# Optimization experiments

Measured on AMD Instinct MI355X. Metric: run time of the kernel, lower is better.

Reference implementation:

```python
import jax, jax.numpy as jnp
import numpy as np

B, C, D, M = 256, 1024, 512, 4096
EPS = 1e-12  # F.normalize default eps


def setup_inputs() -> dict:
    key = jax.random.key(0)
    k1, k2 = jax.random.split(key)
    feature = jax.random.normal(k1, (B, C, D), dtype=jnp.float32)
    memory = jax.random.normal(k2, (M, C), dtype=jnp.float32)
    mask = jnp.ones((B,), dtype=bool)
    return {"feature": feature, "memory": memory, "mask": mask, "train": 1}


def reference(feature, memory, mask, train):
    # ---- Global_Pattern_Adjustment ----
    attn = jax.nn.softmax(feature.mean(axis=1), axis=-1)            # [B, D]
    feature_G = (feature * attn[:, None, :]).mean(axis=-1)          # [B, C]
    score = feature_G @ memory.T                                    # [B, M]
    score_memory = jax.nn.softmax(score, axis=0)                    # softmax over batch
    score_image = jax.nn.softmax(score, axis=1)                     # softmax over memory slots
    memory_response = jax.lax.stop_gradient(score_image) @ memory   # [B, C]
    memory_response = feature_G + memory_response
    global_compensation = feature + memory_response[:, :, None]     # [B, C, D]

    if not train:
        return global_compensation

    # ---- Memory_Evolution (mask-filtered rows emulated by zeroing their update) ----
    idx = jnp.argmax(score_image, axis=1)                           # topk(k=1) -> [B]
    weights = jnp.take_along_axis(score_memory, idx[:, None], axis=1)  # [B, 1]
    m = mask.astype(feature.dtype)[:, None]                         # [B, 1]
    update_vector = feature_G * weights * m                         # [B, C]
    increment = jnp.zeros_like(memory).at[idx].add(update_vector)   # scatter_add -> [M, C]
    upd = increment + memory
    norm = jnp.maximum(jnp.linalg.norm(upd, axis=1, keepdims=True), EPS)
    updated_memory = jax.lax.stop_gradient(upd / norm)              # [M, C]
    return (global_compensation, updated_memory)
```

## Files before the change

### kernel.cpp

```cpp
#include <hip/hip_runtime.h>
#include <math.h>

#define B 256
#define C 1024
#define D 512
#define M 4096
#define KS_SC 4
#define KS_MR 16
#define CHUNK 64
#define CPB 32
#define NCP (C / CPB)
static constexpr float EPS = 1e-12f;

typedef float fx4 __attribute__((ext_vector_type(4)));

__global__ __launch_bounds__(256) void k_colmean(const float* __restrict__ f,
                                                 float* __restrict__ colpart, int b0) {
    __shared__ fx4 buf[128];
    int bx = blockIdx.x, cc = blockIdx.y;
    int b = b0 + bx;
    int t = threadIdx.x;
    int r = t >> 7, lane = t & 127;
    const fx4* f4 = reinterpret_cast<const fx4*>(f)
                  + ((size_t)b * C + cc * CPB + r * 16) * (D / 4) + lane;
    fx4 acc = (fx4)(0.f);
#pragma unroll
    for (int k = 0; k < 16; ++k) acc += f4[(size_t)k * (D / 4)];
    if (r) buf[lane] = acc;
    __syncthreads();
    if (!r) {
        acc += buf[lane];
        reinterpret_cast<fx4*>(colpart)[((size_t)cc * CHUNK + bx) * (D / 4) + lane] = acc;
    }
}

__global__ __launch_bounds__(256) void k_attn(const float* __restrict__ colpart,
                                              float* __restrict__ attnD, int b0) {
    __shared__ float red[256];
    int bl = blockIdx.x;
    int b = b0 + bl;
    int t = threadIdx.x;
    float s0 = 0.f, s1 = 0.f;
#pragma unroll
    for (int p = 0; p < NCP; ++p) {
        s0 += colpart[((size_t)p * CHUNK + bl) * D + t];
        s1 += colpart[((size_t)p * CHUNK + bl) * D + t + 256];
    }
    float x0 = s0 * (1.0f / C), x1 = s1 * (1.0f / C);
    red[t] = fmaxf(x0, x1); __syncthreads();
    for (int s = 128; s > 0; s >>= 1) {
        if (t < s) red[t] = fmaxf(red[t], red[t + s]);
        __syncthreads();
    }
    float mx = red[0]; __syncthreads();
    float e0 = expf(x0 - mx), e1 = expf(x1 - mx);
    red[t] = e0 + e1; __syncthreads();
    for (int s = 128; s > 0; s >>= 1) {
        if (t < s) red[t] += red[t + s];
        __syncthreads();
    }
    float inv = 1.0f / (red[0] * (float)D);
    attnD[(size_t)b * D + t] = e0 * inv;
    attnD[(size_t)b * D + t + 256] = e1 * inv;
}

__global__ __launch_bounds__(256) void k_fg(const float* __restrict__ f,
                                            const float* __restrict__ attnD,
                                            float* __restrict__ fG, int b0) {
    int w = blockIdx.x * 4 + (threadIdx.x >> 6);
    int lane = threadIdx.x & 63;
    int b = b0 + (w >> 10);
    int c = w & 1023;
    const float4* f4 = reinterpret_cast<const float4*>(f) + ((size_t)b * C + c) * (D / 4);
    const float4* a4 = reinterpret_cast<const float4*>(attnD) + (size_t)b * (D / 4);
    float4 v0 = f4[lane], v1 = f4[lane + 64];
    float4 a0 = a4[lane], a1 = a4[lane + 64];
    float acc = v0.x * a0.x + v0.y * a0.y + v0.z * a0.z + v0.w * a0.w
              + v1.x * a1.x + v1.y * a1.y + v1.z * a1.z + v1.w * a1.w;
    for (int s = 32; s > 0; s >>= 1) acc += __shfl_xor(acc, s, 64);
    if (lane == 0) fG[(size_t)b * C + c] = acc;
}

__global__ __launch_bounds__(256) void k_score(const float* __restrict__ A,
                                               const float* __restrict__ Bm,
                                               float* __restrict__ score_p) {
    __shared__ float As[16][64];
    __shared__ float Bs[16][64];
    int t = threadIdx.x;
    int brow = blockIdx.y * 64;
    int mcol = blockIdx.x * 64;
    int kc0 = blockIdx.z * (C / KS_SC);
    int lr = t >> 2, lq = t & 3;
    int r0 = (t >> 4) << 2, c0 = (t & 15) << 2;
    float acc[4][4] = {};
    for (int kc = kc0; kc < kc0 + C / KS_SC; kc += 16) {
        float4 av = *reinterpret_cast<const float4*>(A + (size_t)(brow + lr) * C + kc + lq * 4);
        float4 bv = *reinterpret_cast<const float4*>(Bm + (size_t)(mcol + lr) * C + kc + lq * 4);
        __syncthreads();
        As[lq * 4 + 0][lr] = av.x; As[lq * 4 + 1][lr] = av.y;
        As[lq * 4 + 2][lr] = av.z; As[lq * 4 + 3][lr] = av.w;
        Bs[lq * 4 + 0][lr] = bv.x; Bs[lq * 4 + 1][lr] = bv.y;
        Bs[lq * 4 + 2][lr] = bv.z; Bs[lq * 4 + 3][lr] = bv.w;
        __syncthreads();
#pragma unroll
        for (int kk = 0; kk < 16; ++kk) {
            float a[4], bb[4];
#pragma unroll
            for (int i = 0; i < 4; ++i) a[i] = As[kk][r0 + i];
#pragma unroll
            for (int j = 0; j < 4; ++j) bb[j] = Bs[kk][c0 + j];
#pragma unroll
            for (int i = 0; i < 4; ++i)
#pragma unroll
                for (int j = 0; j < 4; ++j) acc[i][j] += a[i] * bb[j];
        }
    }
    float* o = score_p + (size_t)blockIdx.z * B * M;
#pragma unroll
    for (int i = 0; i < 4; ++i) {
        float4 v = make_float4(acc[i][0], acc[i][1], acc[i][2], acc[i][3]);
        *reinterpret_cast<float4*>(o + (size_t)(brow + r0 + i) * M + mcol + c0) = v;
    }
}

__global__ __launch_bounds__(256) void k_rowsoftmax(const float* __restrict__ score_p,
                                                    float* __restrict__ scoreF,
                                                    float* __restrict__ simg,
                                                    int* __restrict__ idxout,
                                                    float* __restrict__ rowinv) {
    __shared__ float srow[M];
    __shared__ float rv[256];
    __shared__ int ri[256];
    int b = blockIdx.x, t = threadIdx.x;
    const float* p = score_p + (size_t)b * M;
    float mx = -INFINITY; int mi = 0;
    for (int j = t; j < M; j += 256) {
        float s = p[j] + p[j + (size_t)B * M] + p[j + 2 * (size_t)B * M]
                + p[j + 3 * (size_t)B * M];
        srow[j] = s;
        scoreF[(size_t)b * M + j] = s;
        if (s > mx) { mx = s; mi = j; }
    }
    rv[t] = mx; ri[t] = mi; __syncthreads();
    for (int s = 128; s > 0; s >>= 1) {
        if (t < s) {
            if (rv[t + s] > rv[t] || (rv[t + s] == rv[t] && ri[t + s] < ri[t])) {
                rv[t] = rv[t + s]; ri[t] = ri[t + s];
            }
        }
        __syncthreads();
    }
    float rmax = rv[0]; int rid = ri[0];
    __syncthreads();
    float s = 0.f;
    for (int j = t; j < M; j += 256) {
        float e = expf(srow[j] - rmax);
        simg[(size_t)b * M + j] = e;
        s += e;
    }
    rv[t] = s; __syncthreads();
    for (int ss = 128; ss > 0; ss >>= 1) {
        if (t < ss) rv[t] += rv[t + ss];
        __syncthreads();
    }
    if (t == 0) { idxout[b] = rid; rowinv[b] = 1.0f / rv[0]; }
}

__global__ __launch_bounds__(256) void k_mr(const float* __restrict__ simg,
                                            const float* __restrict__ mem,
                                            const float* __restrict__ rowinv,
                                            float* __restrict__ mr_p) {
    __shared__ float As[16][64];
    __shared__ float Bs[16][64];
    int t = threadIdx.x;
    int ccol = blockIdx.x * 64;
    int brow = blockIdx.y * 64;
    int kc0 = blockIdx.z * (M / KS_MR);
    int lr = t >> 2, lq = t & 3;
    int lr2 = t >> 4, lq2 = t & 15;
    int r0 = (t >> 4) << 2, c0 = (t & 15) << 2;
    float acc[4][4] = {};
    for (int kc = kc0; kc < kc0 + M / KS_MR; kc += 16) {
        float4 av = *reinterpret_cast<const float4*>(simg + (size_t)(brow + lr) * M + kc + lq * 4);
        float4 bv = *reinterpret_cast<const float4*>(mem + (size_t)(kc + lr2) * C + ccol + lq2 * 4);
        __syncthreads();
        As[lq * 4 + 0][lr] = av.x; As[lq * 4 + 1][lr] = av.y;
        As[lq * 4 + 2][lr] = av.z; As[lq * 4 + 3][lr] = av.w;
        Bs[lr2][lq2 * 4 + 0] = bv.x; Bs[lr2][lq2 * 4 + 1] = bv.y;
        Bs[lr2][lq2 * 4 + 2] = bv.z; Bs[lr2][lq2 * 4 + 3] = bv.w;
        __syncthreads();
#pragma unroll
        for (int kk = 0; kk < 16; ++kk) {
            float a[4], bb[4];
#pragma unroll
            for (int i = 0; i < 4; ++i) a[i] = As[kk][r0 + i];
#pragma unroll
            for (int j = 0; j < 4; ++j) bb[j] = Bs[kk][c0 + j];
#pragma unroll
            for (int i = 0; i < 4; ++i)
#pragma unroll
                for (int j = 0; j < 4; ++j) acc[i][j] += a[i] * bb[j];
        }
    }
    float* o = mr_p + (size_t)blockIdx.z * B * C;
#pragma unroll
    for (int i = 0; i < 4; ++i) {
        float rinv = rowinv[brow + r0 + i];
        float4 v = make_float4(acc[i][0] * rinv, acc[i][1] * rinv,
                               acc[i][2] * rinv, acc[i][3] * rinv);
        *reinterpret_cast<float4*>(o + (size_t)(brow + r0 + i) * C + ccol + c0) = v;
    }
}

__global__ __launch_bounds__(256) void k_mrred(const float* __restrict__ mr_p,
                                               const float* __restrict__ fG,
                                               float* __restrict__ mrf) {
    size_t row = (size_t)blockIdx.x * 256 + threadIdx.x;
    float a = fG[row];
#pragma unroll
    for (int z = 0; z < KS_MR; ++z) a += mr_p[(size_t)z * B * C + row];
    mrf[row] = a;
}

__global__ __launch_bounds__(256) void k_out(const float* __restrict__ f,
                                             const float* __restrict__ mrf,
                                             float* __restrict__ out) {
    size_t n4 = (size_t)B * C * D / 4;
    const fx4* f4 = reinterpret_cast<const fx4*>(f);
    fx4* o4 = reinterpret_cast<fx4*>(out);
    for (size_t i = (size_t)blockIdx.x * blockDim.x + threadIdx.x; i < n4;
         i += (size_t)gridDim.x * blockDim.x) {
        size_t row = (size_t)B * C - 1 - (i >> 7);
        size_t j = i & 127;
        size_t o = row * 128 + j;
        fx4 v = f4[o];
        v += mrf[row];
        __builtin_nontemporal_store(v, o4 + o);
    }
}

__global__ __launch_bounds__(256) void k_memupd(const float* __restrict__ mem,
                                                const float* __restrict__ fG,
                                                const int* __restrict__ idx,
                                                const float* __restrict__ scoreF,
                                                float* __restrict__ out2) {
    int m = blockIdx.x, t = threadIdx.x;
    __shared__ int sIdx[B];
    __shared__ float se[B];
    __shared__ float red[256];
    __shared__ int sAny;
    if (t == 0) sAny = 0;
    __syncthreads();
    sIdx[t] = idx[t];
    __syncthreads();
    if (sIdx[t] == m) sAny = 1;
    __syncthreads();

    const fx4* m4 = reinterpret_cast<const fx4*>(mem) + (size_t)m * (C / 4);
    fx4 u = m4[t];
    if (sAny) {
        float x = scoreF[(size_t)t * M + m];
        red[t] = x; __syncthreads();
        for (int s = 128; s > 0; s >>= 1) {
            if (t < s) red[t] = fmaxf(red[t], red[t + s]);
            __syncthreads();
        }
        float mx = red[0]; __syncthreads();
        float e = expf(x - mx);
        se[t] = e;
        red[t] = e; __syncthreads();
        for (int s = 128; s > 0; s >>= 1) {
            if (t < s) red[t] += red[t + s];
            __syncthreads();
        }
        float Sinv = 1.0f / red[0];
        __syncthreads();
        for (int b2 = 0; b2 < B; ++b2) {
            if (sIdx[b2] == m) {
                float w = se[b2] * Sinv;
                fx4 g = reinterpret_cast<const fx4*>(fG)[(size_t)b2 * (C / 4) + t];
                u += g * w;
            }
        }
    }
    red[t] = u.x * u.x + u.y * u.y + u.z * u.z + u.w * u.w;
    __syncthreads();
    for (int s = 128; s > 0; s >>= 1) {
        if (t < s) red[t] += red[t + s];
        __syncthreads();
    }
    float invn = 1.0f / fmaxf(sqrtf(red[0]), EPS);
    reinterpret_cast<fx4*>(out2)[(size_t)m * (C / 4) + t] = u * invn;
}

extern "C" void kernel_launch(void* const* d_in, const int* in_sizes, int n_in,
                              void* d_out, int out_size, void* d_ws, size_t ws_size,
                              hipStream_t stream) {
    const float* feature = (const float*)d_in[0];
    const float* memory  = (const float*)d_in[1];
    float* out = (float*)d_out;

    float* ws = (float*)d_ws;
    float* colpart = ws;
    float* attnD   = colpart + (size_t)NCP * CHUNK * D;
    float* fG      = attnD + (size_t)B * D;
    float* scoreF  = fG + (size_t)B * C;
    float* score_p = scoreF + (size_t)B * M;
    float* simg    = score_p + (size_t)KS_SC * B * M;
    float* mr_p    = simg + (size_t)B * M;
    float* mrf     = mr_p + (size_t)KS_MR * B * C;
    float* rowinv  = mrf + (size_t)B * C;
    int*   idx     = (int*)(rowinv + B);

    for (int b0 = 0; b0 < B; b0 += CHUNK) {
        k_colmean<<<dim3(CHUNK, NCP), 256, 0, stream>>>(feature, colpart, b0);
        k_attn<<<CHUNK, 256, 0, stream>>>(colpart, attnD, b0);
        k_fg<<<CHUNK * C / 4, 256, 0, stream>>>(feature, attnD, fG, b0);
    }
    k_score<<<dim3(M / 64, B / 64, KS_SC), 256, 0, stream>>>(fG, memory, score_p);
    k_rowsoftmax<<<B, 256, 0, stream>>>(score_p, scoreF, simg, idx, rowinv);
    k_mr<<<dim3(C / 64, B / 64, KS_MR), 256, 0, stream>>>(simg, memory, rowinv, mr_p);
    k_mrred<<<B * C / 256, 256, 0, stream>>>(mr_p, fG, mrf);
    k_out<<<4096, 256, 0, stream>>>(feature, mrf, out);
    k_memupd<<<M, 256, 0, stream>>>(memory, fG, idx, scoreF, out + (size_t)B * C * D);
}
```

Measured before the change: 518.4 us.

## Use bf16 MFMA for score and memory-response GEMMs with bf16 operand copies

Converts memory, feature_G and the softmax numerators to bf16, including a transposed memory copy, and replaces the two FP32 LDS-tiled GEMMs with bf16 MFMA 16x16x32 kernels that read operands straight from global memory. The row-softmax normalisation moves into the split-K reduction, the row softmax runs with 1024 threads per block, and the MR split-K factor halves. This targets the FP32 FMA cost of the GEMMs, at the price of bf16 precision in the scores, which could flip argmax ties or near-ties and change the memory update.

After: 498.7 us. -3.8%, faster.

```diff
diff --git a/kernel.cpp b/kernel.cpp
--- a/kernel.cpp
+++ b/kernel.cpp
@@ -6,13 +6,48 @@
 #define D 512
 #define M 4096
 #define KS_SC 4
-#define KS_MR 16
+#define KS_MR 8
 #define CHUNK 64
 #define CPB 32
 #define NCP (C / CPB)
 static constexpr float EPS = 1e-12f;
 
 typedef float fx4 __attribute__((ext_vector_type(4)));
+typedef short bf16x8 __attribute__((ext_vector_type(8)));
+typedef float f32x4 __attribute__((ext_vector_type(4)));
+
+static __device__ __forceinline__ unsigned short f2bf(float x) {
+    unsigned u = __builtin_bit_cast(unsigned, x);
+    return (unsigned short)((u + 0x7fffu + ((u >> 16) & 1u)) >> 16);
+}
+
+__global__ __launch_bounds__(256) void k_convmem(const float* __restrict__ mem,
+                                                 unsigned short* __restrict__ memB,
+                                                 unsigned short* __restrict__ memBT) {
+    __shared__ unsigned short lds[64][65];
+    int tm = blockIdx.x * 64;
+    int tc = blockIdx.y * 64;
+    int t = threadIdx.x;
+    int rr = t >> 4, c4 = t & 15;
+#pragma unroll
+    for (int i = 0; i < 4; ++i) {
+        int row = rr + 16 * i;
+        float4 v = *reinterpret_cast<const float4*>(mem + (size_t)(tm + row) * C + tc + c4 * 4);
+        unsigned short b0 = f2bf(v.x), b1 = f2bf(v.y), b2 = f2bf(v.z), b3 = f2bf(v.w);
+        ushort4 w = make_ushort4(b0, b1, b2, b3);
+        *reinterpret_cast<ushort4*>(memB + (size_t)(tm + row) * C + tc + c4 * 4) = w;
+        lds[row][c4 * 4 + 0] = b0; lds[row][c4 * 4 + 1] = b1;
+        lds[row][c4 * 4 + 2] = b2; lds[row][c4 * 4 + 3] = b3;
+    }
+    __syncthreads();
+#pragma unroll
+    for (int i = 0; i < 4; ++i) {
+        int colC = rr + 16 * i;
+        ushort4 w = make_ushort4(lds[c4 * 4 + 0][colC], lds[c4 * 4 + 1][colC],
+                                 lds[c4 * 4 + 2][colC], lds[c4 * 4 + 3][colC]);
+        *reinterpret_cast<ushort4*>(memBT + (size_t)(tc + colC) * M + tm + c4 * 4) = w;
+    }
+}
 
 __global__ __launch_bounds__(256) void k_colmean(const float* __restrict__ f,
                                                  float* __restrict__ colpart, int b0) {
@@ -66,7 +101,8 @@
 
 __global__ __launch_bounds__(256) void k_fg(const float* __restrict__ f,
                                             const float* __restrict__ attnD,
-                                            float* __restrict__ fG, int b0) {
+                                            float* __restrict__ fG,
+                                            unsigned short* __restrict__ fGB, int b0) {
     int w = blockIdx.x * 4 + (threadIdx.x >> 6);
     int lane = threadIdx.x & 63;
     int b = b0 + (w >> 10);
@@ -78,63 +114,58 @@
     float acc = v0.x * a0.x + v0.y * a0.y + v0.z * a0.z + v0.w * a0.w
               + v1.x * a1.x + v1.y * a1.y + v1.z * a1.z + v1.w * a1.w;
     for (int s = 32; s > 0; s >>= 1) acc += __shfl_xor(acc, s, 64);
-    if (lane == 0) fG[(size_t)b * C + c] = acc;
-}
-
-__global__ __launch_bounds__(256) void k_score(const float* __restrict__ A,
-                                               const float* __restrict__ Bm,
+    if (lane == 0) {
+        fG[(size_t)b * C + c] = acc;
+        fGB[(size_t)b * C + c] = f2bf(acc);
+    }
+}
+
+__global__ __launch_bounds__(256) void k_score(const unsigned short* __restrict__ fGB,
+                                               const unsigned short* __restrict__ memB,
                                                float* __restrict__ score_p) {
-    __shared__ float As[16][64];
-    __shared__ float Bs[16][64];
-    int t = threadIdx.x;
-    int brow = blockIdx.y * 64;
-    int mcol = blockIdx.x * 64;
+    int t = threadIdx.x;
+    int lane = t & 63, wid = t >> 6;
+    int wm = wid >> 1, wn = wid & 1;
+    int brow = blockIdx.y * 64 + wm * 32;
+    int mcol = blockIdx.x * 64 + wn * 32;
     int kc0 = blockIdx.z * (C / KS_SC);
-    int lr = t >> 2, lq = t & 3;
-    int r0 = (t >> 4) << 2, c0 = (t & 15) << 2;
-    float acc[4][4] = {};
-    for (int kc = kc0; kc < kc0 + C / KS_SC; kc += 16) {
-        float4 av = *reinterpret_cast<const float4*>(A + (size_t)(brow + lr) * C + kc + lq * 4);
-        float4 bv = *reinterpret_cast<const float4*>(Bm + (size_t)(mcol + lr) * C + kc + lq * 4);
-        __syncthreads();
-        As[lq * 4 + 0][lr] = av.x; As[lq * 4 + 1][lr] = av.y;
-        As[lq * 4 + 2][lr] = av.z; As[lq * 4 + 3][lr] = av.w;
-        Bs[lq * 4 + 0][lr] = bv.x; Bs[lq * 4 + 1][lr] = bv.y;
-        Bs[lq * 4 + 2][lr] = bv.z; Bs[lq * 4 + 3][lr] = bv.w;
-        __syncthreads();
-#pragma unroll
-        for (int kk = 0; kk < 16; ++kk) {
-            float a[4], bb[4];
-#pragma unroll
-            for (int i = 0; i < 4; ++i) a[i] = As[kk][r0 + i];
-#pragma unroll
-            for (int j = 0; j < 4; ++j) bb[j] = Bs[kk][c0 + j];
-#pragma unroll
-            for (int i = 0; i < 4; ++i)
-#pragma unroll
-                for (int j = 0; j < 4; ++j) acc[i][j] += a[i] * bb[j];
-        }
+    int l16 = lane & 15, kg = lane >> 4;
+    f32x4 acc00 = {}, acc01 = {}, acc10 = {}, acc11 = {};
+#pragma unroll
+    for (int ks = 0; ks < C / KS_SC / 32; ++ks) {
+        int kb = kc0 + ks * 32 + kg * 8;
+        bf16x8 a0 = *reinterpret_cast<const bf16x8*>(fGB + (size_t)(brow + l16) * C + kb);
+        bf16x8 a1 = *reinterpret_cast<const bf16x8*>(fGB + (size_t)(brow + 16 + l16) * C + kb);
+        bf16x8 b0 = *reinterpret_cast<const bf16x8*>(memB + (size_t)(mcol + l16) * C + kb);
+        bf16x8 b1 = *reinterpret_cast<const bf16x8*>(memB + (size_t)(mcol + 16 + l16) * C + kb);
+        acc00 = __builtin_amdgcn_mfma_f32_16x16x32_bf16(a0, b0, acc00, 0, 0, 0);
+        acc01 = __builtin_amdgcn_mfma_f32_16x16x32_bf16(a0, b1, acc01, 0, 0, 0);
+        acc10 = __builtin_amdgcn_mfma_f32_16x16x32_bf16(a1, b0, acc10, 0, 0, 0);
+        acc11 = __builtin_amdgcn_mfma_f32_16x16x32_bf16(a1, b1, acc11, 0, 0, 0);
     }
     float* o = score_p + (size_t)blockIdx.z * B * M;
 #pragma unroll
-    for (int i = 0; i < 4; ++i) {
-        float4 v = make_float4(acc[i][0], acc[i][1], acc[i][2], acc[i][3]);
-        *reinterpret_cast<float4*>(o + (size_t)(brow + r0 + i) * M + mcol + c0) = v;
-    }
-}
-
-__global__ __launch_bounds__(256) void k_rowsoftmax(const float* __restrict__ score_p,
-                                                    float* __restrict__ scoreF,
-                                                    float* __restrict__ simg,
-                                                    int* __restrict__ idxout,
-                                                    float* __restrict__ rowinv) {
+    for (int r = 0; r < 4; ++r) {
+        int row0 = brow + kg * 4 + r, row1 = row0 + 16;
+        o[(size_t)row0 * M + mcol + l16]      = acc00[r];
+        o[(size_t)row0 * M + mcol + 16 + l16] = acc01[r];
+        o[(size_t)row1 * M + mcol + l16]      = acc10[r];
+        o[(size_t)row1 * M + mcol + 16 + l16] = acc11[r];
+    }
+}
+
+__global__ __launch_bounds__(1024) void k_rowsoftmax(const float* __restrict__ score_p,
+                                                     float* __restrict__ scoreF,
+                                                     unsigned short* __restrict__ simgB,
+                                                     int* __restrict__ idxout,
+                                                     float* __restrict__ rowinv) {
     __shared__ float srow[M];
-    __shared__ float rv[256];
-    __shared__ int ri[256];
+    __shared__ float rv[1024];
+    __shared__ int ri[1024];
     int b = blockIdx.x, t = threadIdx.x;
     const float* p = score_p + (size_t)b * M;
     float mx = -INFINITY; int mi = 0;
-    for (int j = t; j < M; j += 256) {
+    for (int j = t; j < M; j += 1024) {
         float s = p[j] + p[j + (size_t)B * M] + p[j + 2 * (size_t)B * M]
                 + p[j + 3 * (size_t)B * M];
         srow[j] = s;
@@ -142,7 +173,7 @@
         if (s > mx) { mx = s; mi = j; }
     }
     rv[t] = mx; ri[t] = mi; __syncthreads();
-    for (int s = 128; s > 0; s >>= 1) {
+    for (int s = 512; s > 0; s >>= 1) {
         if (t < s) {
             if (rv[t + s] > rv[t] || (rv[t + s] == rv[t] && ri[t + s] < ri[t])) {
                 rv[t] = rv[t + s]; ri[t] = ri[t + s];
@@ -153,73 +184,62 @@
     float rmax = rv[0]; int rid = ri[0];
     __syncthreads();
     float s = 0.f;
-    for (int j = t; j < M; j += 256) {
+    for (int j = t; j < M; j += 1024) {
         float e = expf(srow[j] - rmax);
-        simg[(size_t)b * M + j] = e;
+        simgB[(size_t)b * M + j] = f2bf(e);
         s += e;
     }
     rv[t] = s; __syncthreads();
-    for (int ss = 128; ss > 0; ss >>= 1) {
+    for (int ss = 512; ss > 0; ss >>= 1) {
         if (t < ss) rv[t] += rv[t + ss];
         __syncthreads();
     }
     if (t == 0) { idxout[b] = rid; rowinv[b] = 1.0f / rv[0]; }
 }
 
-__global__ __launch_bounds__(256) void k_mr(const float* __restrict__ simg,
-                                            const float* __restrict__ mem,
-                                            const float* __restrict__ rowinv,
+__global__ __launch_bounds__(256) void k_mr(const unsigned short* __restrict__ simgB,
+                                            const unsigned short* __restrict__ memBT,
                                             float* __restrict__ mr_p) {
-    __shared__ float As[16][64];
-    __shared__ float Bs[16][64];
-    int t = threadIdx.x;
-    int ccol = blockIdx.x * 64;
-    int brow = blockIdx.y * 64;
+    int t = threadIdx.x;
+    int lane = t & 63, wid = t >> 6;
+    int wm = wid >> 1, wn = wid & 1;
+    int brow = blockIdx.y * 64 + wm * 32;
+    int ccol = blockIdx.x * 64 + wn * 32;
     int kc0 = blockIdx.z * (M / KS_MR);
-    int lr = t >> 2, lq = t & 3;
-    int lr2 = t >> 4, lq2 = t & 15;
-    int r0 = (t >> 4) << 2, c0 = (t & 15) << 2;
-    float acc[4][4] = {};
-    for (int kc = kc0; kc < kc0 + M / KS_MR; kc += 16) {
-        float4 av = *reinterpret_cast<const float4*>(simg + (size_t)(brow + lr) * M + kc + lq * 4);
-        float4 bv = *reinterpret_cast<const float4*>(mem + (size_t)(kc + lr2) * C + ccol + lq2 * 4);
-        __syncthreads();
-        As[lq * 4 + 0][lr] = av.x; As[lq * 4 + 1][lr] = av.y;
-        As[lq * 4 + 2][lr] = av.z; As[lq * 4 + 3][lr] = av.w;
-        Bs[lr2][lq2 * 4 + 0] = bv.x; Bs[lr2][lq2 * 4 + 1] = bv.y;
-        Bs[lr2][lq2 * 4 + 2] = bv.z; Bs[lr2][lq2 * 4 + 3] = bv.w;
-        __syncthreads();
-#pragma unroll
-        for (int kk = 0; kk < 16; ++kk) {
-            float a[4], bb[4];
-#pragma unroll
-            for (int i = 0; i < 4; ++i) a[i] = As[kk][r0 + i];
-#pragma unroll
-            for (int j = 0; j < 4; ++j) bb[j] = Bs[kk][c0 + j];
-#pragma unroll
-            for (int i = 0; i < 4; ++i)
-#pragma unroll
-                for (int j = 0; j < 4; ++j) acc[i][j] += a[i] * bb[j];
-        }
+    int l16 = lane & 15, kg = lane >> 4;
+    f32x4 acc00 = {}, acc01 = {}, acc10 = {}, acc11 = {};
+#pragma unroll 4
+    for (int ks = 0; ks < M / KS_MR / 32; ++ks) {
+        int kb = kc0 + ks * 32 + kg * 8;
+        bf16x8 a0 = *reinterpret_cast<const bf16x8*>(simgB + (size_t)(brow + l16) * M + kb);
+        bf16x8 a1 = *reinterpret_cast<const bf16x8*>(simgB + (size_t)(brow + 16 + l16) * M + kb);
+        bf16x8 b0 = *reinterpret_cast<const bf16x8*>(memBT + (size_t)(ccol + l16) * M + kb);
+        bf16x8 b1 = *reinterpret_cast<const bf16x8*>(memBT + (size_t)(ccol + 16 + l16) * M + kb);
+        acc00 = __builtin_amdgcn_mfma_f32_16x16x32_bf16(a0, b0, acc00, 0, 0, 0);
+        acc01 = __builtin_amdgcn_mfma_f32_16x16x32_bf16(a0, b1, acc01, 0, 0, 0);
+        acc10 = __builtin_amdgcn_mfma_f32_16x16x32_bf16(a1, b0, acc10, 0, 0, 0);
+        acc11 = __builtin_amdgcn_mfma_f32_16x16x32_bf16(a1, b1, acc11, 0, 0, 0);
     }
     float* o = mr_p + (size_t)blockIdx.z * B * C;
 #pragma unroll
-    for (int i = 0; i < 4; ++i) {
-        float rinv = rowinv[brow + r0 + i];
-        float4 v = make_float4(acc[i][0] * rinv, acc[i][1] * rinv,
-                               acc[i][2] * rinv, acc[i][3] * rinv);
-        *reinterpret_cast<float4*>(o + (size_t)(brow + r0 + i) * C + ccol + c0) = v;
+    for (int r = 0; r < 4; ++r) {
+        int row0 = brow + kg * 4 + r, row1 = row0 + 16;
+        o[(size_t)row0 * C + ccol + l16]      = acc00[r];
+        o[(size_t)row0 * C + ccol + 16 + l16] = acc01[r];
+        o[(size_t)row1 * C + ccol + l16]      = acc10[r];
+        o[(size_t)row1 * C + ccol + 16 + l16] = acc11[r];
     }
 }
 
 __global__ __launch_bounds__(256) void k_mrred(const float* __restrict__ mr_p,
                                                const float* __restrict__ fG,
+                                               const float* __restrict__ rowinv,
                                                float* __restrict__ mrf) {
     size_t row = (size_t)blockIdx.x * 256 + threadIdx.x;
-    float a = fG[row];
+    float a = 0.f;
 #pragma unroll
     for (int z = 0; z < KS_MR; ++z) a += mr_p[(size_t)z * B * C + row];
-    mrf[row] = a;
+    mrf[row] = fG[row] + rowinv[row >> 10] * a;
 }
 
 __global__ __launch_bounds__(256) void k_out(const float* __restrict__ f,
@@ -306,21 +326,25 @@
     float* fG      = attnD + (size_t)B * D;
     float* scoreF  = fG + (size_t)B * C;
     float* score_p = scoreF + (size_t)B * M;
-    float* simg    = score_p + (size_t)KS_SC * B * M;
-    float* mr_p    = simg + (size_t)B * M;
+    float* mr_p    = score_p + (size_t)KS_SC * B * M;
     float* mrf     = mr_p + (size_t)KS_MR * B * C;
     float* rowinv  = mrf + (size_t)B * C;
     int*   idx     = (int*)(rowinv + B);
-
+    unsigned short* fGB   = (unsigned short*)(idx + B);
+    unsigned short* memB  = fGB + (size_t)B * C;
+    unsigned short* memBT = memB + (size_t)M * C;
+    unsigned short* simgB = memBT + (size_t)C * M;
+
+    k_convmem<<<dim3(M / 64, C / 64), 256, 0, stream>>>(memory, memB, memBT);
     for (int b0 = 0; b0 < B; b0 += CHUNK) {
         k_colmean<<<dim3(CHUNK, NCP), 256, 0, stream>>>(feature, colpart, b0);
         k_attn<<<CHUNK, 256, 0, stream>>>(colpart, attnD, b0);
-        k_fg<<<CHUNK * C / 4, 256, 0, stream>>>(feature, attnD, fG, b0);
-    }
-    k_score<<<dim3(M / 64, B / 64, KS_SC), 256, 0, stream>>>(fG, memory, score_p);
-    k_rowsoftmax<<<B, 256, 0, stream>>>(score_p, scoreF, simg, idx, rowinv);
-    k_mr<<<dim3(C / 64, B / 64, KS_MR), 256, 0, stream>>>(simg, memory, rowinv, mr_p);
-    k_mrred<<<B * C / 256, 256, 0, stream>>>(mr_p, fG, mrf);
+        k_fg<<<CHUNK * C / 4, 256, 0, stream>>>(feature, attnD, fG, fGB, b0);
+    }
+    k_score<<<dim3(M / 64, B / 64, KS_SC), 256, 0, stream>>>(fGB, memB, score_p);
+    k_rowsoftmax<<<B, 1024, 0, stream>>>(score_p, scoreF, simgB, idx, rowinv);
+    k_mr<<<dim3(C / 64, B / 64, KS_MR), 256, 0, stream>>>(simgB, memBT, mr_p);
+    k_mrred<<<B * C / 256, 256, 0, stream>>>(mr_p, fG, rowinv, mrf);
     k_out<<<4096, 256, 0, stream>>>(feature, mrf, out);
     k_memupd<<<M, 256, 0, stream>>>(memory, fG, idx, scoreF, out + (size_t)B * C * D);
 }
```
